# Kernel optimization log

Hardware: AMD Instinct MI355X
Metric: run time of the kernel (lower is better)

## Reference

```python
import jax, jax.numpy as jnp
import numpy as np
from jax import lax

SEQ_LEN = 256
INPUT_DIM = 4096
NUM_HIDDEN = 2048
NUM_CLASSES = 10


def setup_inputs() -> dict:
    key = jax.random.key(0)
    ks = jax.random.split(key, 4)
    # small-scale random params instead of the degenerate ones-init so tanh is not saturated
    x = jax.random.normal(ks[0], (SEQ_LEN, INPUT_DIM), dtype=jnp.float32)
    W_hx = jax.random.normal(ks[1], (INPUT_DIM, NUM_HIDDEN), dtype=jnp.float32) * 0.01
    W_hh = jax.random.normal(ks[2], (NUM_HIDDEN, NUM_HIDDEN), dtype=jnp.float32) * 0.01
    W_ph = jax.random.normal(ks[3], (NUM_HIDDEN, NUM_CLASSES), dtype=jnp.float32) * 0.01
    b_h = jnp.zeros((NUM_HIDDEN,), dtype=jnp.float32)
    b_p = jnp.zeros((NUM_CLASSES,), dtype=jnp.float32)
    return {"x": x, "W_hx": W_hx, "W_hh": W_hh, "W_ph": W_ph, "b_h": b_h, "b_p": b_p}


def reference(x, W_hx, W_hh, W_ph, b_h, b_p):
    # Precompute the input projections for all timesteps: [S, H]
    xw = x @ W_hx
    H = W_hh.shape[0]
    # Faithful to the torch code: initial hidden state is an [H, H] MATRIX,
    # and the per-step [H]-vector input term broadcasts over its rows.
    h0 = jnp.zeros((H, H), dtype=x.dtype)

    def step(h, xw_t):
        # h: [H, H]; xw_t: [H] broadcasts over rows
        h_new = jnp.tanh(xw_t + h @ W_hh + b_h)
        return h_new, None

    h_final, _ = lax.scan(step, h0, xw)
    p = h_final @ W_ph + b_p            # [H, C]
    return jax.nn.softmax(jnp.sum(p, axis=0), axis=0)  # [C]
```

## Files before the change

### kernel.cpp

```cpp
#include <hip/hip_runtime.h>
#include <hip/hip_bf16.h>
#include <hip/hip_cooperative_groups.h>

#define SEQ 256
#define IND 4096
#define HID 2048
#define NCLS 10
#define NBLK 256
#define COLS 8

__global__ __launch_bounds__(256) void xw_gemm2(const float* __restrict__ A,
                                                const float* __restrict__ B,
                                                float* __restrict__ C) {
    __shared__ float As[32][33];
    __shared__ float Bs[32][64];
    const int bm = blockIdx.y * 32;
    const int bn = blockIdx.x * 64;
    const int tid = threadIdx.x;
    const int tx = tid & 15;
    const int ty = tid >> 4;

    float acc[2][4] = {};

    for (int k0 = 0; k0 < IND; k0 += 32) {
        {
            const int ar = tid >> 3;
            const int kq = (tid & 7) * 4;
            const float4 a4 = *reinterpret_cast<const float4*>(
                &A[(size_t)(bm + ar) * IND + k0 + kq]);
            As[kq + 0][ar] = a4.x;
            As[kq + 1][ar] = a4.y;
            As[kq + 2][ar] = a4.z;
            As[kq + 3][ar] = a4.w;
        }
        {
            const int kr = tid >> 4;
            const int cq = (tid & 15) * 4;
            *reinterpret_cast<float4*>(&Bs[kr][cq]) =
                *reinterpret_cast<const float4*>(&B[(size_t)(k0 + kr) * HID + bn + cq]);
            *reinterpret_cast<float4*>(&Bs[kr + 16][cq]) =
                *reinterpret_cast<const float4*>(&B[(size_t)(k0 + kr + 16) * HID + bn + cq]);
        }
        __syncthreads();

        #pragma unroll
        for (int kk = 0; kk < 32; ++kk) {
            const float a0 = As[kk][ty * 2 + 0];
            const float a1 = As[kk][ty * 2 + 1];
            const float4 b4 = *reinterpret_cast<const float4*>(&Bs[kk][tx * 4]);
            acc[0][0] += a0 * b4.x; acc[0][1] += a0 * b4.y;
            acc[0][2] += a0 * b4.z; acc[0][3] += a0 * b4.w;
            acc[1][0] += a1 * b4.x; acc[1][1] += a1 * b4.y;
            acc[1][2] += a1 * b4.z; acc[1][3] += a1 * b4.w;
        }
        __syncthreads();
    }

    #pragma unroll
    for (int i = 0; i < 2; ++i) {
        float4 cv = make_float4(acc[i][0], acc[i][1], acc[i][2], acc[i][3]);
        *reinterpret_cast<float4*>(
            &C[(size_t)(bm + ty * 2 + i) * HID + bn + tx * 4]) = cv;
    }
}

__global__ __launch_bounds__(256, 1) void rnn_v4(const float* __restrict__ W,
                                                 const float* __restrict__ xwg,
                                                 const float* __restrict__ b_h,
                                                 unsigned long long* __restrict__ buf,
                                                 float* __restrict__ v_out) {
    const int b = blockIdx.x;
    const int tid = threadIdx.x;
    const int gbase = b * COLS;
    const int col = tid & 7;
    const int seg = tid >> 3;
    const int wid = tid >> 6;
    const int lane = tid & 63;

    __shared__ float Wf[16 * 32 * COLS * 4];
    __shared__ float v2[16 * 32 * 4];
    __shared__ float red[4][COLS];

    for (int chunk = 0; chunk < 16; ++chunk) {
        const int r = chunk * 128 + (tid >> 1);
        const int c4 = (tid & 1) * 4;
        const float4 w4 = *reinterpret_cast<const float4*>(
            &W[(size_t)r * HID + gbase + c4]);
        const int i = (r >> 2) & 15, sg = r >> 6, e = r & 3;
        const float vls[4] = {w4.x, w4.y, w4.z, w4.w};
        #pragma unroll
        for (int j = 0; j < 4; ++j)
            Wf[(((i * 32 + sg) * COLS) + c4 + j) * 4 + e] = vls[j];
    }
    float bias = 0.0f;
    if (tid < COLS) bias = b_h[gbase + tid];
    __syncthreads();

    for (int t = 0; t < SEQ; ++t) {
        float xwv = 0.0f;
        if (tid < COLS) xwv = xwg[(size_t)t * HID + gbase + tid];

        if (t > 0) {
            const unsigned long long* bb = buf + (size_t)(t & 1) * HID;
            const unsigned tg = (unsigned)t;
            for (;;) {
                unsigned long long w[8];
                #pragma unroll
                for (int k = 0; k < 8; ++k)
                    w[k] = __hip_atomic_load(&bb[k * 256 + tid],
                                             __ATOMIC_RELAXED,
                                             __HIP_MEMORY_SCOPE_AGENT);
                bool ok = true;
                #pragma unroll
                for (int k = 0; k < 8; ++k)
                    ok &= ((unsigned)(w[k] >> 32) == tg);
                if (ok) {
                    #pragma unroll
                    for (int k = 0; k < 8; ++k) {
                        const int r = k * 256 + tid;
                        const int i = (r >> 2) & 15, sg = r >> 6, e = r & 3;
                        const int bw = (i * 128 + sg * 4) ^ ((i & 7) << 2);
                        v2[bw + e] = __uint_as_float((unsigned)w[k]);
                    }
                    break;
                }
            }
        } else {
            #pragma unroll
            for (int k = 0; k < 8; ++k) v2[k * 256 + tid] = 0.0f;
        }
        __syncthreads();

        float acc = 0.0f;
        #pragma unroll
        for (int i = 0; i < 16; ++i) {
            const float4 wq = *reinterpret_cast<const float4*>(
                &Wf[((i * 32 + seg) * COLS + col) * 4]);
            const int vb = (i * 128 + seg * 4) ^ ((i & 7) << 2);
            const float4 vq = *reinterpret_cast<const float4*>(&v2[vb]);
            acc += wq.x * vq.x + wq.y * vq.y + wq.z * vq.z + wq.w * vq.w;
        }
        acc += __shfl_xor(acc, 8, 64);
        acc += __shfl_xor(acc, 16, 64);
        acc += __shfl_xor(acc, 32, 64);
        if (lane < COLS) red[wid][lane] = acc;
        __syncthreads();

        if (tid < COLS) {
            const float s = xwv + bias
                          + red[0][tid] + red[1][tid] + red[2][tid] + red[3][tid];
            const float h = tanhf(s);
            const unsigned long long pk =
                ((unsigned long long)(unsigned)(t + 1) << 32) |
                (unsigned long long)__float_as_uint(h);
            __hip_atomic_store(&buf[(size_t)((t + 1) & 1) * HID + gbase + tid],
                               pk, __ATOMIC_RELAXED, __HIP_MEMORY_SCOPE_AGENT);
            if (t == SEQ - 1) v_out[gbase + tid] = h;
        }
    }
}

__global__ __launch_bounds__(256) void final_kernel(const float* __restrict__ v,
                                                    const float* __restrict__ W_ph,
                                                    const float* __restrict__ b_p,
                                                    float* __restrict__ out) {
    __shared__ float red[256][NCLS];
    const int tid = threadIdx.x;
    float acc[NCLS] = {};
    for (int jj = tid; jj < HID; jj += 256) {
        const float vj = v[jj];
        #pragma unroll
        for (int cdx = 0; cdx < NCLS; ++cdx)
            acc[cdx] += vj * W_ph[jj * NCLS + cdx];
    }
    #pragma unroll
    for (int cdx = 0; cdx < NCLS; ++cdx) red[tid][cdx] = acc[cdx];
    __syncthreads();
    for (int sft = 128; sft > 0; sft >>= 1) {
        if (tid < sft) {
            #pragma unroll
            for (int cdx = 0; cdx < NCLS; ++cdx)
                red[tid][cdx] += red[tid + sft][cdx];
        }
        __syncthreads();
    }
    if (tid == 0) {
        float logits[NCLS];
        float m = -1e30f;
        #pragma unroll
        for (int cdx = 0; cdx < NCLS; ++cdx) {
            logits[cdx] = (float)HID * (red[0][cdx] + b_p[cdx]);
            m = fmaxf(m, logits[cdx]);
        }
        float den = 0.0f, e[NCLS];
        #pragma unroll
        for (int cdx = 0; cdx < NCLS; ++cdx) {
            e[cdx] = expf(logits[cdx] - m);
            den += e[cdx];
        }
        #pragma unroll
        for (int cdx = 0; cdx < NCLS; ++cdx) out[cdx] = e[cdx] / den;
    }
}

extern "C" void kernel_launch(void* const* d_in, const int* in_sizes, int n_in,
                              void* d_out, int out_size, void* d_ws, size_t ws_size,
                              hipStream_t stream) {
    const float* x    = (const float*)d_in[0];
    const float* W_hx = (const float*)d_in[1];
    const float* W_hh = (const float*)d_in[2];
    const float* W_ph = (const float*)d_in[3];
    const float* b_h  = (const float*)d_in[4];
    const float* b_p  = (const float*)d_in[5];
    float* out = (float*)d_out;

    float* xw               = (float*)d_ws;
    unsigned long long* buf = (unsigned long long*)(xw + (size_t)SEQ * HID);
    float* v                = (float*)(buf + 2 * HID);

    dim3 g1(HID / 64, SEQ / 32);
    xw_gemm2<<<g1, 256, 0, stream>>>(x, W_hx, xw);

    {
        const float* whh_a = W_hh;
        const float* xw_a  = xw;
        const float* bh_a  = b_h;
        unsigned long long* buf_a = buf;
        float* v_a = v;
        void* args[] = {(void*)&whh_a, (void*)&xw_a, (void*)&bh_a,
                        (void*)&buf_a, (void*)&v_a};
        hipLaunchCooperativeKernel((const void*)rnn_v4, dim3(NBLK), dim3(256),
                                   args, 0, stream);
    }

    final_kernel<<<1, 256, 0, stream>>>(v, W_ph, b_p, out);
}
```

Measured before the change: 819.9 us.

## Fuse projection GEMM, recurrence and classifier into one cooperative megakernel

```diff
diff --git a/kernel.cpp b/kernel.cpp
--- a/kernel.cpp
+++ b/kernel.cpp
@@ -8,198 +8,224 @@
 #define NCLS 10
 #define NBLK 256
 #define COLS 8
-
-__global__ __launch_bounds__(256) void xw_gemm2(const float* __restrict__ A,
-                                                const float* __restrict__ B,
-                                                float* __restrict__ C) {
-    __shared__ float As[32][33];
-    __shared__ float Bs[32][64];
-    const int bm = blockIdx.y * 32;
-    const int bn = blockIdx.x * 64;
-    const int tid = threadIdx.x;
-    const int tx = tid & 15;
-    const int ty = tid >> 4;
-
-    float acc[2][4] = {};
-
-    for (int k0 = 0; k0 < IND; k0 += 32) {
-        {
-            const int ar = tid >> 3;
-            const int kq = (tid & 7) * 4;
-            const float4 a4 = *reinterpret_cast<const float4*>(
-                &A[(size_t)(bm + ar) * IND + k0 + kq]);
-            As[kq + 0][ar] = a4.x;
-            As[kq + 1][ar] = a4.y;
-            As[kq + 2][ar] = a4.z;
-            As[kq + 3][ar] = a4.w;
-        }
-        {
-            const int kr = tid >> 4;
-            const int cq = (tid & 15) * 4;
-            *reinterpret_cast<float4*>(&Bs[kr][cq]) =
-                *reinterpret_cast<const float4*>(&B[(size_t)(k0 + kr) * HID + bn + cq]);
-            *reinterpret_cast<float4*>(&Bs[kr + 16][cq]) =
-                *reinterpret_cast<const float4*>(&B[(size_t)(k0 + kr + 16) * HID + bn + cq]);
-        }
-        __syncthreads();
-
-        #pragma unroll
-        for (int kk = 0; kk < 32; ++kk) {
-            const float a0 = As[kk][ty * 2 + 0];
-            const float a1 = As[kk][ty * 2 + 1];
-            const float4 b4 = *reinterpret_cast<const float4*>(&Bs[kk][tx * 4]);
-            acc[0][0] += a0 * b4.x; acc[0][1] += a0 * b4.y;
-            acc[0][2] += a0 * b4.z; acc[0][3] += a0 * b4.w;
-            acc[1][0] += a1 * b4.x; acc[1][1] += a1 * b4.y;
-            acc[1][2] += a1 * b4.z; acc[1][3] += a1 * b4.w;
-        }
-        __syncthreads();
-    }
-
-    #pragma unroll
-    for (int i = 0; i < 2; ++i) {
-        float4 cv = make_float4(acc[i][0], acc[i][1], acc[i][2], acc[i][3]);
-        *reinterpret_cast<float4*>(
-            &C[(size_t)(bm + ty * 2 + i) * HID + bn + tx * 4]) = cv;
-    }
-}
-
-__global__ __launch_bounds__(256, 1) void rnn_v4(const float* __restrict__ W,
-                                                 const float* __restrict__ xwg,
-                                                 const float* __restrict__ b_h,
-                                                 unsigned long long* __restrict__ buf,
-                                                 float* __restrict__ v_out) {
+#define TAGX 0x7E57A55Au
+
+__global__ __launch_bounds__(256, 1) void mega(const float* __restrict__ x,
+                                               const float* __restrict__ W_hx,
+                                               const float* __restrict__ W_hh,
+                                               const float* __restrict__ W_ph,
+                                               const float* __restrict__ b_h,
+                                               const float* __restrict__ b_p,
+                                               unsigned long long* __restrict__ xwt,
+                                               unsigned long long* __restrict__ buf,
+                                               float* __restrict__ out) {
+    __shared__ float smem[18496];
     const int b = blockIdx.x;
     const int tid = threadIdx.x;
-    const int gbase = b * COLS;
-    const int col = tid & 7;
-    const int seg = tid >> 3;
-    const int wid = tid >> 6;
-    const int lane = tid & 63;
-
-    __shared__ float Wf[16 * 32 * COLS * 4];
-    __shared__ float v2[16 * 32 * 4];
-    __shared__ float red[4][COLS];
-
-    for (int chunk = 0; chunk < 16; ++chunk) {
-        const int r = chunk * 128 + (tid >> 1);
-        const int c4 = (tid & 1) * 4;
-        const float4 w4 = *reinterpret_cast<const float4*>(
-            &W[(size_t)r * HID + gbase + c4]);
-        const int i = (r >> 2) & 15, sg = r >> 6, e = r & 3;
-        const float vls[4] = {w4.x, w4.y, w4.z, w4.w};
-        #pragma unroll
-        for (int j = 0; j < 4; ++j)
-            Wf[(((i * 32 + sg) * COLS) + c4 + j) * 4 + e] = vls[j];
+
+    {
+        float* As = smem;
+        float* Bs = smem + 1056;
+        const int bm = (b >> 5) * 32;
+        const int bn = (b & 31) * 64;
+        const int tx = tid & 15;
+        const int ty = tid >> 4;
+        float acc[2][4] = {};
+
+        for (int k0 = 0; k0 < IND; k0 += 32) {
+            {
+                const int ar = tid >> 3;
+                const int kq = (tid & 7) * 4;
+                const float4 a4 = *reinterpret_cast<const float4*>(
+                    &x[(size_t)(bm + ar) * IND + k0 + kq]);
+                As[(kq + 0) * 33 + ar] = a4.x;
+                As[(kq + 1) * 33 + ar] = a4.y;
+                As[(kq + 2) * 33 + ar] = a4.z;
+                As[(kq + 3) * 33 + ar] = a4.w;
+            }
+            {
+                const int kr = tid >> 4;
+                const int cq = (tid & 15) * 4;
+                *reinterpret_cast<float4*>(&Bs[kr * 64 + cq]) =
+                    *reinterpret_cast<const float4*>(&W_hx[(size_t)(k0 + kr) * HID + bn + cq]);
+                *reinterpret_cast<float4*>(&Bs[(kr + 16) * 64 + cq]) =
+                    *reinterpret_cast<const float4*>(&W_hx[(size_t)(k0 + kr + 16) * HID + bn + cq]);
+            }
+            __syncthreads();
+            #pragma unroll
+            for (int kk = 0; kk < 32; ++kk) {
+                const float a0 = As[kk * 33 + ty * 2 + 0];
+                const float a1 = As[kk * 33 + ty * 2 + 1];
+                const float4 b4 = *reinterpret_cast<const float4*>(&Bs[kk * 64 + tx * 4]);
+                acc[0][0] += a0 * b4.x; acc[0][1] += a0 * b4.y;
+                acc[0][2] += a0 * b4.z; acc[0][3] += a0 * b4.w;
+                acc[1][0] += a1 * b4.x; acc[1][1] += a1 * b4.y;
+                acc[1][2] += a1 * b4.z; acc[1][3] += a1 * b4.w;
+            }
+            __syncthreads();
+        }
+        #pragma unroll
+        for (int i = 0; i < 2; ++i)
+            #pragma unroll
+            for (int j = 0; j < 4; ++j) {
+                const int row = bm + ty * 2 + i;
+                const int cc = bn + tx * 4 + j;
+                const unsigned long long pk =
+                    ((unsigned long long)TAGX << 32) |
+                    (unsigned long long)__float_as_uint(acc[i][j]);
+                __hip_atomic_store(&xwt[(size_t)row * HID + cc], pk,
+                                   __ATOMIC_RELAXED, __HIP_MEMORY_SCOPE_AGENT);
+            }
     }
-    float bias = 0.0f;
-    if (tid < COLS) bias = b_h[gbase + tid];
     __syncthreads();
 
-    for (int t = 0; t < SEQ; ++t) {
-        float xwv = 0.0f;
-        if (tid < COLS) xwv = xwg[(size_t)t * HID + gbase + tid];
-
-        if (t > 0) {
-            const unsigned long long* bb = buf + (size_t)(t & 1) * HID;
-            const unsigned tg = (unsigned)t;
-            for (;;) {
+    {
+        float* Wf  = smem;
+        float* v2  = smem + 16384;
+        float* red = smem + 18432;
+
+        const int gbase = b * COLS;
+        const int col = tid & 7;
+        const int seg = tid >> 3;
+        const int wid = tid >> 6;
+        const int lane = tid & 63;
+        const int rb = wid * 512 + lane;
+
+        for (int chunk = 0; chunk < 16; ++chunk) {
+            const int r = chunk * 128 + (tid >> 1);
+            const int c4 = (tid & 1) * 4;
+            const float4 w4 = *reinterpret_cast<const float4*>(
+                &W_hh[(size_t)r * HID + gbase + c4]);
+            const int i = (r >> 2) & 15, sg = r >> 6, e = r & 3;
+            const float vls[4] = {w4.x, w4.y, w4.z, w4.w};
+            #pragma unroll
+            for (int j = 0; j < 4; ++j)
+                Wf[(((i * 32 + sg) * COLS) + c4 + j) * 4 + e] = vls[j];
+        }
+        const float bias = (tid < COLS) ? b_h[gbase + tid] : 0.0f;
+        __syncthreads();
+
+        for (int t = 0; t < SEQ; ++t) {
+            unsigned long long xwv_u = 0;
+            if (tid < COLS)
+                xwv_u = __hip_atomic_load(&xwt[(size_t)t * HID + gbase + tid],
+                                          __ATOMIC_RELAXED, __HIP_MEMORY_SCOPE_AGENT);
+
+            if (t > 0) {
+                const unsigned long long* bb = buf + (size_t)(t & 1) * HID;
+                const unsigned tg = (unsigned)t;
                 unsigned long long w[8];
+                for (;;) {
+                    #pragma unroll
+                    for (int k = 0; k < 8; ++k)
+                        w[k] = __hip_atomic_load(&bb[rb + k * 64],
+                                                 __ATOMIC_RELAXED,
+                                                 __HIP_MEMORY_SCOPE_AGENT);
+                    bool ok = true;
+                    #pragma unroll
+                    for (int k = 0; k < 8; ++k)
+                        ok &= ((unsigned)(w[k] >> 32) == tg);
+                    if (ok) break;
+                }
                 #pragma unroll
-                for (int k = 0; k < 8; ++k)
-                    w[k] = __hip_atomic_load(&bb[k * 256 + tid],
-                                             __ATOMIC_RELAXED,
-                                             __HIP_MEMORY_SCOPE_AGENT);
-                bool ok = true;
+                for (int k = 0; k < 8; ++k) {
+                    const int r = rb + k * 64;
+                    const int i = (r >> 2) & 15, sg = r >> 6, e = r & 3;
+                    const int bw = (i * 128 + sg * 4) ^ ((i & 7) << 2);
+                    v2[bw + e] = __uint_as_float((unsigned)w[k]);
+                }
+            } else {
                 #pragma unroll
-                for (int k = 0; k < 8; ++k)
-                    ok &= ((unsigned)(w[k] >> 32) == tg);
-                if (ok) {
-                    #pragma unroll
-                    for (int k = 0; k < 8; ++k) {
-                        const int r = k * 256 + tid;
-                        const int i = (r >> 2) & 15, sg = r >> 6, e = r & 3;
-                        const int bw = (i * 128 + sg * 4) ^ ((i & 7) << 2);
-                        v2[bw + e] = __uint_as_float((unsigned)w[k]);
-                    }
-                    break;
+                for (int k = 0; k < 8; ++k) {
+                    const int r = rb + k * 64;
+                    const int i = (r >> 2) & 15, sg = r >> 6, e = r & 3;
+                    const int bw = (i * 128 + sg * 4) ^ ((i & 7) << 2);
+                    v2[bw + e] = 0.0f;
                 }
             }
-        } else {
-            #pragma unroll
-            for (int k = 0; k < 8; ++k) v2[k * 256 + tid] = 0.0f;
-        }
+
+            float acc = 0.0f;
+            #pragma unroll
+            for (int i = 0; i < 16; ++i) {
+                const float4 wq = *reinterpret_cast<const float4*>(
+                    &Wf[((i * 32 + seg) * COLS + col) * 4]);
+                const int vb = (i * 128 + seg * 4) ^ ((i & 7) << 2);
+                const float4 vq = *reinterpret_cast<const float4*>(&v2[vb]);
+                acc += wq.x * vq.x + wq.y * vq.y + wq.z * vq.z + wq.w * vq.w;
+            }
+            acc += __shfl_xor(acc, 8, 64);
+            acc += __shfl_xor(acc, 16, 64);
+            acc += __shfl_xor(acc, 32, 64);
+            if (lane < COLS) red[(t & 1) * 32 + wid * 8 + lane] = acc;
+            __syncthreads();
+
+            if (tid < COLS) {
+                while ((unsigned)(xwv_u >> 32) != TAGX)
+                    xwv_u = __hip_atomic_load(&xwt[(size_t)t * HID + gbase + tid],
+                                              __ATOMIC_RELAXED,
+                                              __HIP_MEMORY_SCOPE_AGENT);
+                const float* rp = red + (t & 1) * 32;
+                const float s = __uint_as_float((unsigned)xwv_u) + bias
+                              + rp[tid] + rp[8 + tid] + rp[16 + tid] + rp[24 + tid];
+                const float h = tanhf(s);
+                const unsigned long long pk =
+                    ((unsigned long long)(unsigned)(t + 1) << 32) |
+                    (unsigned long long)__float_as_uint(h);
+                __hip_atomic_store(&buf[(size_t)((t + 1) & 1) * HID + gbase + tid],
+                                   pk, __ATOMIC_RELAXED, __HIP_MEMORY_SCOPE_AGENT);
+            }
+        }
+    }
+
+    if (b == 0) {
         __syncthreads();
-
-        float acc = 0.0f;
-        #pragma unroll
-        for (int i = 0; i < 16; ++i) {
-            const float4 wq = *reinterpret_cast<const float4*>(
-                &Wf[((i * 32 + seg) * COLS + col) * 4]);
-            const int vb = (i * 128 + seg * 4) ^ ((i & 7) << 2);
-            const float4 vq = *reinterpret_cast<const float4*>(&v2[vb]);
-            acc += wq.x * vq.x + wq.y * vq.y + wq.z * vq.z + wq.w * vq.w;
-        }
-        acc += __shfl_xor(acc, 8, 64);
-        acc += __shfl_xor(acc, 16, 64);
-        acc += __shfl_xor(acc, 32, 64);
-        if (lane < COLS) red[wid][lane] = acc;
+        float vv[8];
+        #pragma unroll
+        for (int k = 0; k < 8; ++k) {
+            unsigned long long w;
+            do {
+                w = __hip_atomic_load(&buf[k * 256 + tid],
+                                      __ATOMIC_RELAXED, __HIP_MEMORY_SCOPE_AGENT);
+            } while ((unsigned)(w >> 32) != (unsigned)SEQ);
+            vv[k] = __uint_as_float((unsigned)w);
+        }
+        float a10[NCLS] = {};
+        #pragma unroll
+        for (int k = 0; k < 8; ++k) {
+            const int r = k * 256 + tid;
+            #pragma unroll
+            for (int c = 0; c < NCLS; ++c)
+                a10[c] += vv[k] * W_ph[(size_t)r * NCLS + c];
+        }
+        float* fred = smem;
+        #pragma unroll
+        for (int c = 0; c < NCLS; ++c) fred[tid * NCLS + c] = a10[c];
         __syncthreads();
-
-        if (tid < COLS) {
-            const float s = xwv + bias
-                          + red[0][tid] + red[1][tid] + red[2][tid] + red[3][tid];
-            const float h = tanhf(s);
-            const unsigned long long pk =
-                ((unsigned long long)(unsigned)(t + 1) << 32) |
-                (unsigned long long)__float_as_uint(h);
-            __hip_atomic_store(&buf[(size_t)((t + 1) & 1) * HID + gbase + tid],
-                               pk, __ATOMIC_RELAXED, __HIP_MEMORY_SCOPE_AGENT);
-            if (t == SEQ - 1) v_out[gbase + tid] = h;
-        }
-    }
-}
-
-__global__ __launch_bounds__(256) void final_kernel(const float* __restrict__ v,
-                                                    const float* __restrict__ W_ph,
-                                                    const float* __restrict__ b_p,
-                                                    float* __restrict__ out) {
-    __shared__ float red[256][NCLS];
-    const int tid = threadIdx.x;
-    float acc[NCLS] = {};
-    for (int jj = tid; jj < HID; jj += 256) {
-        const float vj = v[jj];
-        #pragma unroll
-        for (int cdx = 0; cdx < NCLS; ++cdx)
-            acc[cdx] += vj * W_ph[jj * NCLS + cdx];
-    }
-    #pragma unroll
-    for (int cdx = 0; cdx < NCLS; ++cdx) red[tid][cdx] = acc[cdx];
-    __syncthreads();
-    for (int sft = 128; sft > 0; sft >>= 1) {
-        if (tid < sft) {
-            #pragma unroll
-            for (int cdx = 0; cdx < NCLS; ++cdx)
-                red[tid][cdx] += red[tid + sft][cdx];
-        }
-        __syncthreads();
-    }
-    if (tid == 0) {
-        float logits[NCLS];
-        float m = -1e30f;
-        #pragma unroll
-        for (int cdx = 0; cdx < NCLS; ++cdx) {
-            logits[cdx] = (float)HID * (red[0][cdx] + b_p[cdx]);
-            m = fmaxf(m, logits[cdx]);
-        }
-        float den = 0.0f, e[NCLS];
-        #pragma unroll
-        for (int cdx = 0; cdx < NCLS; ++cdx) {
-            e[cdx] = expf(logits[cdx] - m);
-            den += e[cdx];
-        }
-        #pragma unroll
-        for (int cdx = 0; cdx < NCLS; ++cdx) out[cdx] = e[cdx] / den;
+        for (int sft = 128; sft > 0; sft >>= 1) {
+            if (tid < sft) {
+                #pragma unroll
+                for (int c = 0; c < NCLS; ++c)
+                    fred[tid * NCLS + c] += fred[(tid + sft) * NCLS + c];
+            }
+            __syncthreads();
+        }
+        if (tid == 0) {
+            float logits[NCLS];
+            float m = -1e30f;
+            #pragma unroll
+            for (int c = 0; c < NCLS; ++c) {
+                logits[c] = (float)HID * (fred[c] + b_p[c]);
+                m = fmaxf(m, logits[c]);
+            }
+            float den = 0.0f, e[NCLS];
+            #pragma unroll
+            for (int c = 0; c < NCLS; ++c) {
+                e[c] = expf(logits[c] - m);
+                den += e[c];
+            }
+            #pragma unroll
+            for (int c = 0; c < NCLS; ++c) out[c] = e[c] / den;
+        }
     }
 }
 
@@ -214,24 +240,16 @@
     const float* b_p  = (const float*)d_in[5];
     float* out = (float*)d_out;
 
-    float* xw               = (float*)d_ws;
-    unsigned long long* buf = (unsigned long long*)(xw + (size_t)SEQ * HID);
-    float* v                = (float*)(buf + 2 * HID);
-
-    dim3 g1(HID / 64, SEQ / 32);
-    xw_gemm2<<<g1, 256, 0, stream>>>(x, W_hx, xw);
-
-    {
-        const float* whh_a = W_hh;
-        const float* xw_a  = xw;
-        const float* bh_a  = b_h;
-        unsigned long long* buf_a = buf;
-        float* v_a = v;
-        void* args[] = {(void*)&whh_a, (void*)&xw_a, (void*)&bh_a,
-                        (void*)&buf_a, (void*)&v_a};
-        hipLaunchCooperativeKernel((const void*)rnn_v4, dim3(NBLK), dim3(256),
-                                   args, 0, stream);
-    }
-
-    final_kernel<<<1, 256, 0, stream>>>(v, W_ph, b_p, out);
+    unsigned long long* xwt = (unsigned long long*)d_ws;
+    unsigned long long* buf = xwt + (size_t)SEQ * HID;
+
+    const float* x_a = x; const float* whx_a = W_hx; const float* whh_a = W_hh;
+    const float* wph_a = W_ph; const float* bh_a = b_h; const float* bp_a = b_p;
+    unsigned long long* xwt_a = xwt; unsigned long long* buf_a = buf;
+    float* out_a = out;
+    void* args[] = {(void*)&x_a, (void*)&whx_a, (void*)&whh_a, (void*)&wph_a,
+                    (void*)&bh_a, (void*)&bp_a, (void*)&xwt_a, (void*)&buf_a,
+                    (void*)&out_a};
+    hipLaunchCooperativeKernel((const void*)mega, dim3(NBLK), dim3(256),
+                               args, 0, stream);
 }
```

New measurement: 797.8 us. 2.7% less time.

## Publish per-wave partial sums and apply tanh at consumers, bf16 recurrent weights

Applied to the files above, without the earlier changes.

```diff
diff --git a/kernel.cpp b/kernel.cpp
--- a/kernel.cpp
+++ b/kernel.cpp
@@ -12,7 +12,7 @@
 __global__ __launch_bounds__(256) void xw_gemm2(const float* __restrict__ A,
                                                 const float* __restrict__ B,
                                                 float* __restrict__ C) {
-    __shared__ float As[32][33];
+    __shared__ float As[32][34];
     __shared__ float Bs[32][64];
     const int bm = blockIdx.y * 32;
     const int bn = blockIdx.x * 64;
@@ -45,13 +45,12 @@
 
         #pragma unroll
         for (int kk = 0; kk < 32; ++kk) {
-            const float a0 = As[kk][ty * 2 + 0];
-            const float a1 = As[kk][ty * 2 + 1];
+            const float2 a01 = *reinterpret_cast<const float2*>(&As[kk][ty * 2]);
             const float4 b4 = *reinterpret_cast<const float4*>(&Bs[kk][tx * 4]);
-            acc[0][0] += a0 * b4.x; acc[0][1] += a0 * b4.y;
-            acc[0][2] += a0 * b4.z; acc[0][3] += a0 * b4.w;
-            acc[1][0] += a1 * b4.x; acc[1][1] += a1 * b4.y;
-            acc[1][2] += a1 * b4.z; acc[1][3] += a1 * b4.w;
+            acc[0][0] += a01.x * b4.x; acc[0][1] += a01.x * b4.y;
+            acc[0][2] += a01.x * b4.z; acc[0][3] += a01.x * b4.w;
+            acc[1][0] += a01.y * b4.x; acc[1][1] += a01.y * b4.y;
+            acc[1][2] += a01.y * b4.z; acc[1][3] += a01.y * b4.w;
         }
         __syncthreads();
     }
@@ -64,123 +63,160 @@
     }
 }
 
-__global__ __launch_bounds__(256, 1) void rnn_v4(const float* __restrict__ W,
+__device__ __forceinline__ unsigned short f2bf(float f) {
+    unsigned u = __float_as_uint(f);
+    u += 0x7fffu + ((u >> 16) & 1u);
+    return (unsigned short)(u >> 16);
+}
+__device__ __forceinline__ float bflo(unsigned u) {
+    return __uint_as_float(u << 16);
+}
+__device__ __forceinline__ float bfhi(unsigned u) {
+    return __uint_as_float(u & 0xffff0000u);
+}
+
+__global__ __launch_bounds__(256, 1) void rnn_v5(const float* __restrict__ W,
                                                  const float* __restrict__ xwg,
                                                  const float* __restrict__ b_h,
-                                                 unsigned long long* __restrict__ buf,
-                                                 float* __restrict__ v_out) {
+                                                 unsigned long long* __restrict__ buf) {
     const int b = blockIdx.x;
     const int tid = threadIdx.x;
     const int gbase = b * COLS;
-    const int col = tid & 7;
-    const int seg = tid >> 3;
+    const int lane = tid & 63;
     const int wid = tid >> 6;
-    const int lane = tid & 63;
-
-    __shared__ float Wf[16 * 32 * COLS * 4];
-    __shared__ float v2[16 * 32 * 4];
-    __shared__ float red[4][COLS];
-
-    for (int chunk = 0; chunk < 16; ++chunk) {
-        const int r = chunk * 128 + (tid >> 1);
-        const int c4 = (tid & 1) * 4;
-        const float4 w4 = *reinterpret_cast<const float4*>(
-            &W[(size_t)r * HID + gbase + c4]);
-        const int i = (r >> 2) & 15, sg = r >> 6, e = r & 3;
-        const float vls[4] = {w4.x, w4.y, w4.z, w4.w};
-        #pragma unroll
-        for (int j = 0; j < 4; ++j)
-            Wf[(((i * 32 + sg) * COLS) + c4 + j) * 4 + e] = vls[j];
-    }
-    float bias = 0.0f;
-    if (tid < COLS) bias = b_h[gbase + tid];
+    const int sl = lane >> 3;
+    const int col = lane & 7;
+    const int seg = wid * 8 + sl;
+
+    __shared__ unsigned short Wfb[8 * 32 * 8 * 8];
+    __shared__ float v2[4 * 512];
+    __shared__ float xl[SEQ * COLS];
+
+    for (int rr = 0; rr < 8; ++rr) {
+        const int r = rr * 256 + tid;
+        const float4 w0 = *reinterpret_cast<const float4*>(&W[(size_t)r * HID + gbase]);
+        const float4 w1 = *reinterpret_cast<const float4*>(&W[(size_t)r * HID + gbase + 4]);
+        const int i = (r >> 3) & 7, sg = r >> 6, e = r & 7;
+        const float wv[8] = {w0.x, w0.y, w0.z, w0.w, w1.x, w1.y, w1.z, w1.w};
+        #pragma unroll
+        for (int c = 0; c < 8; ++c)
+            Wfb[(((i * 32 + sg) * 8) + c) * 8 + e] = f2bf(wv[c]);
+    }
+    for (int ii = 0; ii < 8; ++ii) {
+        const int idx = ii * 256 + tid;
+        xl[idx] = xwg[(size_t)(idx >> 3) * HID + gbase + (idx & 7)];
+    }
+    const float bias = (lane < COLS) ? b_h[gbase + lane] : 0.0f;
+    #pragma unroll
+    for (int k = 0; k < 8; ++k) v2[wid * 512 + k * 64 + lane] = 0.0f;
     __syncthreads();
 
     for (int t = 0; t < SEQ; ++t) {
-        float xwv = 0.0f;
-        if (tid < COLS) xwv = xwg[(size_t)t * HID + gbase + tid];
-
         if (t > 0) {
-            const unsigned long long* bb = buf + (size_t)(t & 1) * HID;
+            const unsigned long long* bp = buf + (size_t)(t & 1) * (HID * 4);
             const unsigned tg = (unsigned)t;
+            unsigned long long wv[8][4];
+            unsigned got = 0;
+            #pragma unroll
+            for (int k = 0; k < 8; ++k) {
+                const unsigned long long* p = bp + (size_t)(wid * 512 + k * 64 + lane) * 4;
+                wv[k][0] = __hip_atomic_load(p + 0, __ATOMIC_RELAXED, __HIP_MEMORY_SCOPE_AGENT);
+                wv[k][1] = __hip_atomic_load(p + 1, __ATOMIC_RELAXED, __HIP_MEMORY_SCOPE_AGENT);
+                wv[k][2] = __hip_atomic_load(p + 2, __ATOMIC_RELAXED, __HIP_MEMORY_SCOPE_AGENT);
+                wv[k][3] = __hip_atomic_load(p + 3, __ATOMIC_RELAXED, __HIP_MEMORY_SCOPE_AGENT);
+            }
             for (;;) {
-                unsigned long long w[8];
                 #pragma unroll
-                for (int k = 0; k < 8; ++k)
-                    w[k] = __hip_atomic_load(&bb[k * 256 + tid],
-                                             __ATOMIC_RELAXED,
-                                             __HIP_MEMORY_SCOPE_AGENT);
-                bool ok = true;
+                for (int k = 0; k < 8; ++k) {
+                    if (!(got & (1u << k))) {
+                        bool ok = true;
+                        #pragma unroll
+                        for (int s = 0; s < 4; ++s)
+                            ok &= ((unsigned)(wv[k][s] >> 32) == tg);
+                        if (ok) {
+                            const float s4 = __uint_as_float((unsigned)wv[k][0])
+                                           + __uint_as_float((unsigned)wv[k][1])
+                                           + __uint_as_float((unsigned)wv[k][2])
+                                           + __uint_as_float((unsigned)wv[k][3]);
+                            const int q = (k * 16 + (lane >> 2)) ^ k;
+                            v2[wid * 512 + q * 4 + (lane & 3)] = tanhf(s4);
+                            got |= (1u << k);
+                        }
+                    }
+                }
+                if (got == 0xFFu) break;
                 #pragma unroll
-                for (int k = 0; k < 8; ++k)
-                    ok &= ((unsigned)(w[k] >> 32) == tg);
-                if (ok) {
-                    #pragma unroll
-                    for (int k = 0; k < 8; ++k) {
-                        const int r = k * 256 + tid;
-                        const int i = (r >> 2) & 15, sg = r >> 6, e = r & 3;
-                        const int bw = (i * 128 + sg * 4) ^ ((i & 7) << 2);
-                        v2[bw + e] = __uint_as_float((unsigned)w[k]);
+                for (int k = 0; k < 8; ++k) {
+                    if (!(got & (1u << k))) {
+                        const unsigned long long* p = bp + (size_t)(wid * 512 + k * 64 + lane) * 4;
+                        wv[k][0] = __hip_atomic_load(p + 0, __ATOMIC_RELAXED, __HIP_MEMORY_SCOPE_AGENT);
+                        wv[k][1] = __hip_atomic_load(p + 1, __ATOMIC_RELAXED, __HIP_MEMORY_SCOPE_AGENT);
+                        wv[k][2] = __hip_atomic_load(p + 2, __ATOMIC_RELAXED, __HIP_MEMORY_SCOPE_AGENT);
+                        wv[k][3] = __hip_atomic_load(p + 3, __ATOMIC_RELAXED, __HIP_MEMORY_SCOPE_AGENT);
                     }
-                    break;
                 }
             }
-        } else {
-            #pragma unroll
-            for (int k = 0; k < 8; ++k) v2[k * 256 + tid] = 0.0f;
         }
         __syncthreads();
 
         float acc = 0.0f;
-        #pragma unroll
-        for (int i = 0; i < 16; ++i) {
-            const float4 wq = *reinterpret_cast<const float4*>(
-                &Wf[((i * 32 + seg) * COLS + col) * 4]);
-            const int vb = (i * 128 + seg * 4) ^ ((i & 7) << 2);
-            const float4 vq = *reinterpret_cast<const float4*>(&v2[vb]);
-            acc += wq.x * vq.x + wq.y * vq.y + wq.z * vq.z + wq.w * vq.w;
+        const int vbase = wid * 512;
+        #pragma unroll
+        for (int i = 0; i < 8; ++i) {
+            const uint4 wq = *reinterpret_cast<const uint4*>(
+                &Wfb[(((i * 32 + seg) * 8) + col) * 8]);
+            const int q0 = (sl * 16 + i * 2) ^ sl;
+            const int q1 = (sl * 16 + i * 2 + 1) ^ sl;
+            const float4 va = *reinterpret_cast<const float4*>(&v2[vbase + q0 * 4]);
+            const float4 vb = *reinterpret_cast<const float4*>(&v2[vbase + q1 * 4]);
+            acc += bflo(wq.x) * va.x + bfhi(wq.x) * va.y
+                 + bflo(wq.y) * va.z + bfhi(wq.y) * va.w
+                 + bflo(wq.z) * vb.x + bfhi(wq.z) * vb.y
+                 + bflo(wq.w) * vb.z + bfhi(wq.w) * vb.w;
         }
         acc += __shfl_xor(acc, 8, 64);
         acc += __shfl_xor(acc, 16, 64);
         acc += __shfl_xor(acc, 32, 64);
-        if (lane < COLS) red[wid][lane] = acc;
-        __syncthreads();
-
-        if (tid < COLS) {
-            const float s = xwv + bias
-                          + red[0][tid] + red[1][tid] + red[2][tid] + red[3][tid];
-            const float h = tanhf(s);
+
+        if (lane < COLS) {
+            const float part = acc + ((wid == 0) ? (xl[t * COLS + lane] + bias) : 0.0f);
             const unsigned long long pk =
                 ((unsigned long long)(unsigned)(t + 1) << 32) |
-                (unsigned long long)__float_as_uint(h);
-            __hip_atomic_store(&buf[(size_t)((t + 1) & 1) * HID + gbase + tid],
+                (unsigned long long)__float_as_uint(part);
+            __hip_atomic_store(&buf[(size_t)((t + 1) & 1) * (HID * 4)
+                                    + (size_t)(gbase + lane) * 4 + wid],
                                pk, __ATOMIC_RELAXED, __HIP_MEMORY_SCOPE_AGENT);
-            if (t == SEQ - 1) v_out[gbase + tid] = h;
-        }
-    }
-}
-
-__global__ __launch_bounds__(256) void final_kernel(const float* __restrict__ v,
-                                                    const float* __restrict__ W_ph,
-                                                    const float* __restrict__ b_p,
-                                                    float* __restrict__ out) {
+        }
+    }
+}
+
+__global__ __launch_bounds__(256) void final_v2(const unsigned long long* __restrict__ buf,
+                                                const float* __restrict__ W_ph,
+                                                const float* __restrict__ b_p,
+                                                float* __restrict__ out) {
     __shared__ float red[256][NCLS];
     const int tid = threadIdx.x;
     float acc[NCLS] = {};
-    for (int jj = tid; jj < HID; jj += 256) {
-        const float vj = v[jj];
-        #pragma unroll
-        for (int cdx = 0; cdx < NCLS; ++cdx)
-            acc[cdx] += vj * W_ph[jj * NCLS + cdx];
+    for (int k = 0; k < 8; ++k) {
+        const int r = k * 256 + tid;
+        const unsigned long long* p = buf + (size_t)r * 4;
+        const float s4 = __uint_as_float((unsigned)p[0])
+                       + __uint_as_float((unsigned)p[1])
+                       + __uint_as_float((unsigned)p[2])
+                       + __uint_as_float((unsigned)p[3]);
+        const float v = tanhf(s4);
+        #pragma unroll
+        for (int c = 0; c < NCLS; ++c)
+            acc[c] += v * W_ph[(size_t)r * NCLS + c];
     }
     #pragma unroll
-    for (int cdx = 0; cdx < NCLS; ++cdx) red[tid][cdx] = acc[cdx];
+    for (int c = 0; c < NCLS; ++c) red[tid][c] = acc[c];
     __syncthreads();
     for (int sft = 128; sft > 0; sft >>= 1) {
         if (tid < sft) {
             #pragma unroll
-            for (int cdx = 0; cdx < NCLS; ++cdx)
-                red[tid][cdx] += red[tid + sft][cdx];
+            for (int c = 0; c < NCLS; ++c)
+                red[tid][c] += red[tid + sft][c];
         }
         __syncthreads();
     }
@@ -188,18 +224,18 @@
         float logits[NCLS];
         float m = -1e30f;
         #pragma unroll
-        for (int cdx = 0; cdx < NCLS; ++cdx) {
-            logits[cdx] = (float)HID * (red[0][cdx] + b_p[cdx]);
-            m = fmaxf(m, logits[cdx]);
+        for (int c = 0; c < NCLS; ++c) {
+            logits[c] = (float)HID * (red[0][c] + b_p[c]);
+            m = fmaxf(m, logits[c]);
         }
         float den = 0.0f, e[NCLS];
         #pragma unroll
-        for (int cdx = 0; cdx < NCLS; ++cdx) {
-            e[cdx] = expf(logits[cdx] - m);
-            den += e[cdx];
-        }
-        #pragma unroll
-        for (int cdx = 0; cdx < NCLS; ++cdx) out[cdx] = e[cdx] / den;
+        for (int c = 0; c < NCLS; ++c) {
+            e[c] = expf(logits[c] - m);
+            den += e[c];
+        }
+        #pragma unroll
+        for (int c = 0; c < NCLS; ++c) out[c] = e[c] / den;
     }
 }
 
@@ -216,7 +252,6 @@
 
     float* xw               = (float*)d_ws;
     unsigned long long* buf = (unsigned long long*)(xw + (size_t)SEQ * HID);
-    float* v                = (float*)(buf + 2 * HID);
 
     dim3 g1(HID / 64, SEQ / 32);
     xw_gemm2<<<g1, 256, 0, stream>>>(x, W_hx, xw);
@@ -226,12 +261,10 @@
         const float* xw_a  = xw;
         const float* bh_a  = b_h;
         unsigned long long* buf_a = buf;
-        float* v_a = v;
-        void* args[] = {(void*)&whh_a, (void*)&xw_a, (void*)&bh_a,
-                        (void*)&buf_a, (void*)&v_a};
-        hipLaunchCooperativeKernel((const void*)rnn_v4, dim3(NBLK), dim3(256),
+        void* args[] = {(void*)&whh_a, (void*)&xw_a, (void*)&bh_a, (void*)&buf_a};
+        hipLaunchCooperativeKernel((const void*)rnn_v5, dim3(NBLK), dim3(256),
                                    args, 0, stream);
     }
 
-    final_kernel<<<1, 256, 0, stream>>>(v, W_ph, b_p, out);
-}
+    final_v2<<<1, 256, 0, stream>>>(buf, W_ph, b_p, out);
+}
```

After: 1.825 ms. +122.7%, slower.
